# Kernel optimization log

Measured on AMD Instinct MI355X. Metric: run time of the kernel, lower is better.

The kernel has to match this reference:

```python
import jax, jax.numpy as jnp
import numpy as np

N = 50000        # nodes
E = 600000       # edges (no self-loops; reference adds N self-loops)
IN_C = 64
OUT_C = 64
HEADS = 2
NEG_SLOPE = 0.2  # GraphLayer default negative_slope
BN_EPS = 1e-5


def setup_inputs() -> dict:
    key = jax.random.key(0)
    ks = jax.random.split(key, 14)
    x = jax.random.normal(ks[0], (N, IN_C), dtype=jnp.float32)
    # edge_index with no self-loops by construction (original calls remove_self_loops)
    src = jax.random.randint(ks[1], (E,), 0, N, dtype=jnp.int32)
    off = jax.random.randint(ks[2], (E,), 1, N, dtype=jnp.int32)
    dst = (src + off) % N
    edge_index = jnp.stack([src, dst])  # [2, E]
    embedding = jax.random.normal(ks[3], (N, OUT_C), dtype=jnp.float32)
    s = 0.1
    lin_w = jax.random.normal(ks[4], (IN_C, HEADS * OUT_C), dtype=jnp.float32) * s
    att_i = jax.random.normal(ks[5], (1, HEADS, OUT_C), dtype=jnp.float32) * s
    att_j = jax.random.normal(ks[6], (1, HEADS, OUT_C), dtype=jnp.float32) * s
    att_em_i = jax.random.normal(ks[7], (1, HEADS, OUT_C), dtype=jnp.float32) * s
    att_em_j = jax.random.normal(ks[8], (1, HEADS, OUT_C), dtype=jnp.float32) * s
    gnn_bias = jnp.zeros((HEADS * OUT_C,), dtype=jnp.float32)
    ff_w = jax.random.normal(ks[9], (HEADS * OUT_C, OUT_C), dtype=jnp.float32) * s
    ff_b = jnp.zeros((OUT_C,), dtype=jnp.float32)
    bn_gamma = jnp.ones((OUT_C,), dtype=jnp.float32)
    bn_beta = jnp.zeros((OUT_C,), dtype=jnp.float32)
    return {"x": x, "edge_index": edge_index, "embedding": embedding,
            "lin_w": lin_w, "att_i": att_i, "att_j": att_j,
            "att_em_i": att_em_i, "att_em_j": att_em_j, "gnn_bias": gnn_bias,
            "ff_w": ff_w, "ff_b": ff_b, "bn_gamma": bn_gamma, "bn_beta": bn_beta}


def reference(x, edge_index, embedding, lin_w, att_i, att_j, att_em_i, att_em_j,
              gnn_bias, ff_w, ff_b, bn_gamma, bn_beta):
    n = x.shape[0]
    h = (x @ lin_w).reshape(n, HEADS, OUT_C)  # lin projection, per-head view
    # add self-loops (input already has none)
    ar = jnp.arange(n, dtype=edge_index.dtype)
    ei = jnp.concatenate([edge_index, jnp.stack([ar, ar])], axis=1)
    src, dst = ei[0], ei[1]                   # x_j = source, x_i = target
    x_i, x_j = h[dst], h[src]                 # [Et, H, C]
    emb_i = embedding[dst][:, None, :]        # [Et, 1, C] broadcast over heads
    emb_j = embedding[src][:, None, :]
    # alpha = <cat(x_i,emb_i), cat(att_i,att_em_i)> + <cat(x_j,emb_j), cat(att_j,att_em_j)>
    alpha = ((x_i * att_i[0]).sum(-1) + (emb_i * att_em_i[0]).sum(-1)
             + (x_j * att_j[0]).sum(-1) + (emb_j * att_em_j[0]).sum(-1))  # [Et, H]
    alpha = jax.nn.leaky_relu(alpha, NEG_SLOPE)
    # segment softmax over incoming edges of each target node (PyG softmax)
    amax = jax.ops.segment_max(alpha, dst, num_segments=n)
    ex = jnp.exp(alpha - amax[dst])
    denom = jax.ops.segment_sum(ex, dst, num_segments=n)
    alpha = ex / (denom[dst] + 1e-16)
    out = jax.ops.segment_sum(x_j * alpha[:, :, None], dst, num_segments=n)  # [n,H,C]
    out = out.reshape(n, HEADS * OUT_C) + gnn_bias  # concat heads + bias
    out = out @ ff_w + ff_b                         # self.ff
    mean = out.mean(axis=0)                          # BatchNorm1d, training stats
    var = out.var(axis=0)                            # biased variance (torch BN)
    out = (out - mean) / jnp.sqrt(var + BN_EPS) * bn_gamma + bn_beta
    return jax.nn.relu(out)
```

## Files before the change

### kernel.cpp

```cpp
#include <hip/hip_runtime.h>

#define C 64
#define HC 128
#define NEG 0.2f

typedef __attribute__((ext_vector_type(8))) short bf16x8;
typedef __attribute__((ext_vector_type(4))) float f32x4;

__device__ __forceinline__ float lrelu(float v) { return v >= 0.f ? v : NEG * v; }
__device__ __forceinline__ unsigned short f2bf(float f) {
    unsigned u = __float_as_uint(f);
    return (unsigned short)((u + 0x7fffu + ((u >> 16) & 1u)) >> 16);
}
__device__ __forceinline__ float bflo(unsigned u) { return __uint_as_float(u << 16); }
__device__ __forceinline__ float bfhi(unsigned u) { return __uint_as_float(u & 0xffff0000u); }

__global__ __launch_bounds__(256) void k1_mfma(
    const float* __restrict__ x, const float* __restrict__ lin_w,
    const float* __restrict__ emb,
    const float* __restrict__ att_i, const float* __restrict__ att_j,
    const float* __restrict__ att_em_i, const float* __restrict__ att_em_j,
    unsigned* __restrict__ hb, float2* __restrict__ a_i2,
    float2* __restrict__ a_j2, int n_nodes)
{
    __shared__ __align__(16) char smem[8192];
    const int t = threadIdx.x;
    const int lane = t & 63, w = t >> 6;
    const int r = lane & 15, g = lane >> 4;

    bf16x8 B[4][2][2];
#pragma unroll
    for (int m4 = 0; m4 < 4; ++m4)
#pragma unroll
        for (int p = 0; p < 2; ++p)
#pragma unroll
            for (int kk = 0; kk < 2; ++kk) {
                bf16x8 bb;
#pragma unroll
                for (int j = 0; j < 8; ++j)
                    bb[j] = (short)f2bf(lin_w[(kk * 32 + 8 * g + j) * HC + 32 * m4 + 2 * r + p]);
                B[m4][p][kk] = bb;
            }
    float wi[4][2], wj[4][2];
#pragma unroll
    for (int m4 = 0; m4 < 4; ++m4)
#pragma unroll
        for (int p = 0; p < 2; ++p) {
            wi[m4][p] = att_i[32 * m4 + 2 * r + p];
            wj[m4][p] = att_j[32 * m4 + 2 * r + p];
        }
    float wem_i0[4], wem_i1[4], wem_j0[4], wem_j1[4];
#pragma unroll
    for (int q = 0; q < 4; ++q) {
        wem_i0[q] = att_em_i[q * 16 + r];
        wem_i1[q] = att_em_i[64 + q * 16 + r];
        wem_j0[q] = att_em_j[q * 16 + r];
        wem_j1[q] = att_em_j[64 + q * 16 + r];
    }

    {
        const int row = t >> 2, q = t & 3;
        const int gn = blockIdx.x * 64 + row;
        float ff[16];
        if (gn < n_nodes) {
            const float4* xs = (const float4*)(x + (size_t)gn * C + q * 16);
            *(float4*)&ff[0] = xs[0]; *(float4*)&ff[4] = xs[1];
            *(float4*)&ff[8] = xs[2]; *(float4*)&ff[12] = xs[3];
        } else {
#pragma unroll
            for (int j = 0; j < 16; ++j) ff[j] = 0.f;
        }
        bf16x8 p0, p1;
#pragma unroll
        for (int j = 0; j < 8; ++j) {
            p0[j] = (short)f2bf(ff[j]);
            p1[j] = (short)f2bf(ff[8 + j]);
        }
        const unsigned bb = (unsigned)((row >> 4) * 2048 + (row & 15) * 128 + q * 32);
        const unsigned sw = (unsigned)((row & 7) << 4);
        *(bf16x8*)(smem + ((bb) ^ sw)) = p0;
        *(bf16x8*)(smem + ((bb + 16) ^ sw)) = p1;
    }
    __syncthreads();

    bf16x8 A[2];
    const unsigned ab = (unsigned)(w * 2048 + r * 128 + g * 16);
    const unsigned sw = (unsigned)((r & 7) << 4);
    A[0] = *(const bf16x8*)(smem + ((ab) ^ sw));
    A[1] = *(const bf16x8*)(smem + ((ab + 64) ^ sw));

    f32x4 acc[4][2];
#pragma unroll
    for (int m4 = 0; m4 < 4; ++m4)
#pragma unroll
        for (int p = 0; p < 2; ++p) acc[m4][p] = (f32x4){0.f, 0.f, 0.f, 0.f};
#pragma unroll
    for (int kk = 0; kk < 2; ++kk)
#pragma unroll
        for (int m4 = 0; m4 < 4; ++m4)
#pragma unroll
            for (int p = 0; p < 2; ++p)
                acc[m4][p] = __builtin_amdgcn_mfma_f32_16x16x32_bf16(A[kk], B[m4][p][kk], acc[m4][p], 0, 0, 0);

    const int nb = blockIdx.x * 64 + w * 16 + 4 * g;
#pragma unroll
    for (int j = 0; j < 4; ++j) {
        const int rr = nb + j;
        if (rr < n_nodes) {
            float pi0 = 0.f, pi1 = 0.f, pj0 = 0.f, pj1 = 0.f;
            unsigned* hp = hb + (size_t)rr * 64 + r;
#pragma unroll
            for (int m4 = 0; m4 < 4; ++m4) {
                const float ev = acc[m4][0][j], ov = acc[m4][1][j];
                hp[m4 * 16] = ((unsigned)f2bf(ov) << 16) | (unsigned)f2bf(ev);
                if (m4 < 2) {
                    pi0 = fmaf(ev, wi[m4][0], fmaf(ov, wi[m4][1], pi0));
                    pj0 = fmaf(ev, wj[m4][0], fmaf(ov, wj[m4][1], pj0));
                } else {
                    pi1 = fmaf(ev, wi[m4][0], fmaf(ov, wi[m4][1], pi1));
                    pj1 = fmaf(ev, wj[m4][0], fmaf(ov, wj[m4][1], pj1));
                }
            }
#pragma unroll
            for (int q = 0; q < 4; ++q) {
                const float ev = emb[(size_t)rr * C + q * 16 + r];
                pi0 = fmaf(ev, wem_i0[q], pi0);
                pi1 = fmaf(ev, wem_i1[q], pi1);
                pj0 = fmaf(ev, wem_j0[q], pj0);
                pj1 = fmaf(ev, wem_j1[q], pj1);
            }
#pragma unroll
            for (int m = 1; m < 16; m <<= 1) {
                pi0 += __shfl_xor(pi0, m, 64);
                pi1 += __shfl_xor(pi1, m, 64);
                pj0 += __shfl_xor(pj0, m, 64);
                pj1 += __shfl_xor(pj1, m, 64);
            }
            if (r == 0) {
                a_i2[rr] = make_float2(pi0, pi1);
                a_j2[rr] = make_float2(pj0, pj1);
            }
        }
    }
}

__global__ __launch_bounds__(256) void k_edge(
    const int* __restrict__ dstv, int* __restrict__ deg,
    int* __restrict__ rank, int e)
{
    int i = blockIdx.x * 256 + threadIdx.x;
    if (i < e) rank[i] = atomicAdd(&deg[dstv[i]], 1);
}

__global__ __launch_bounds__(256) void k_scan(
    const int* __restrict__ deg, int* __restrict__ counter,
    int* __restrict__ rowptr, int n)
{
    __shared__ int sh[256];
    __shared__ int s_base;
    const int t = threadIdx.x;
    const int i0 = blockIdx.x * 512 + t * 2;
    const int a = (i0 < n) ? deg[i0] : 0;
    const int b = (i0 + 1 < n) ? deg[i0 + 1] : 0;
    const int s = a + b;
    sh[t] = s;
    __syncthreads();
    for (int off = 1; off < 256; off <<= 1) {
        int v = (t >= off) ? sh[t - off] : 0;
        __syncthreads();
        sh[t] += v;
        __syncthreads();
    }
    const int excl = sh[t] - s;
    if (t == 255) s_base = atomicAdd(counter, sh[255]);
    __syncthreads();
    const int base = s_base;
    if (i0 < n)     rowptr[i0]     = base + excl;
    if (i0 + 1 < n) rowptr[i0 + 1] = base + excl + a;
}

__global__ __launch_bounds__(256) void k_fill(
    const int* __restrict__ srcv, const int* __restrict__ dstv,
    const int* __restrict__ rank, const int* __restrict__ rowptr,
    int* __restrict__ csr, int e)
{
    int i = blockIdx.x * 256 + threadIdx.x;
    if (i >= e) return;
    csr[rowptr[dstv[i]] + rank[i]] = srcv[i];
}

__global__ __launch_bounds__(256) void k_gather(
    const int* __restrict__ csr, const int* __restrict__ rowptr,
    const int* __restrict__ deg, const unsigned* __restrict__ hb,
    const float2* __restrict__ a_i2, const float2* __restrict__ a_j2,
    const float2* __restrict__ bias2, unsigned* __restrict__ out1b, int n_nodes)
{
    const int lane = threadIdx.x & 63;
    const int n = blockIdx.x * 4 + (threadIdx.x >> 6);
    if (n >= n_nodes) return;
    const int r0 = __builtin_amdgcn_readfirstlane(rowptr[n]);
    const int r1 = r0 + __builtin_amdgcn_readfirstlane(deg[n]);
    const float2 ai = a_i2[n];
    const float2 ajs = a_j2[n];
    const float es0 = __expf(lrelu(ai.x + ajs.x));
    const float es1 = __expf(lrelu(ai.y + ajs.y));
    float den0 = es0, den1 = es1;
    const unsigned hv = hb[(size_t)n * 64 + lane];
    const float exs = (lane < 32) ? es0 : es1;
    float2 acc = make_float2(exs * bflo(hv), exs * bfhi(hv));
#pragma unroll 4
    for (int r = r0; r < r1; ++r) {
        const int se = csr[r];
        const float2 aj = a_j2[se];
        const float ex0 = __expf(lrelu(ai.x + aj.x));
        const float ex1 = __expf(lrelu(ai.y + aj.y));
        den0 += ex0; den1 += ex1;
        const float exh = (lane < 32) ? ex0 : ex1;
        const unsigned v = hb[(size_t)se * 64 + lane];
        acc.x = fmaf(exh, bflo(v), acc.x);
        acc.y = fmaf(exh, bfhi(v), acc.y);
    }
    const float den = (lane < 32) ? den0 : den1;
    const float inv = 1.f / (den + 1e-16f);
    const float2 bv = bias2[lane];
    const unsigned lo = f2bf(fmaf(acc.x, inv, bv.x));
    const unsigned hi = f2bf(fmaf(acc.y, inv, bv.y));
    out1b[(size_t)n * 64 + lane] = (hi << 16) | lo;
}

__global__ __launch_bounds__(256) void k4_ff(
    const unsigned* __restrict__ out1b, const float* __restrict__ ff_w,
    const float* __restrict__ ff_b, float* __restrict__ out2,
    float* __restrict__ colsum, float* __restrict__ colsq, int n_nodes)
{
    __shared__ __align__(16) char smem[16384];
    const int t = threadIdx.x;
    const int lane = t & 63, w = t >> 6;
    const int r = lane & 15, g = lane >> 4;

    bf16x8 B[4][4];
#pragma unroll
    for (int tt = 0; tt < 4; ++tt)
#pragma unroll
        for (int kk = 0; kk < 4; ++kk) {
            bf16x8 bb;
#pragma unroll
            for (int j = 0; j < 8; ++j)
                bb[j] = (short)f2bf(ff_w[(kk * 32 + 8 * g + j) * C + tt * 16 + r]);
            B[tt][kk] = bb;
        }
    float fb[4];
#pragma unroll
    for (int tt = 0; tt < 4; ++tt) fb[tt] = ff_b[tt * 16 + r];

    {
        const int row = t >> 2, q = t & 3;
        const int gn = blockIdx.x * 64 + row;
        uint4 u[4];
        if (gn < n_nodes) {
            const uint4* rs = (const uint4*)(out1b + (size_t)gn * 64 + q * 16);
            u[0] = rs[0]; u[1] = rs[1]; u[2] = rs[2]; u[3] = rs[3];
        } else {
            u[0] = u[1] = u[2] = u[3] = make_uint4(0, 0, 0, 0);
        }
        const unsigned bb = (unsigned)((row >> 4) * 4096 + (row & 15) * 256 + q * 64);
        const unsigned sw = (unsigned)((row & 7) << 4);
#pragma unroll
        for (int i2 = 0; i2 < 4; ++i2)
            *(uint4*)(smem + ((bb + i2 * 16) ^ sw)) = u[i2];
    }
    __syncthreads();

    bf16x8 A[4];
    const unsigned ab = (unsigned)(w * 4096 + r * 256 + g * 16);
    const unsigned sw = (unsigned)((r & 7) << 4);
#pragma unroll
    for (int kk = 0; kk < 4; ++kk)
        A[kk] = *(const bf16x8*)(smem + ((ab + kk * 64) ^ sw));

    f32x4 acc[4];
#pragma unroll
    for (int tt = 0; tt < 4; ++tt) acc[tt] = (f32x4){0.f, 0.f, 0.f, 0.f};
#pragma unroll
    for (int kk = 0; kk < 4; ++kk)
#pragma unroll
        for (int tt = 0; tt < 4; ++tt)
            acc[tt] = __builtin_amdgcn_mfma_f32_16x16x32_bf16(A[kk], B[tt][kk], acc[tt], 0, 0, 0);

    const int nb = blockIdx.x * 64 + w * 16 + 4 * g;
    float st[4] = {0.f, 0.f, 0.f, 0.f}, st2[4] = {0.f, 0.f, 0.f, 0.f};
#pragma unroll
    for (int j = 0; j < 4; ++j) {
        const int rr = nb + j;
        if (rr < n_nodes) {
            float* op = out2 + (size_t)rr * C + r;
#pragma unroll
            for (int tt = 0; tt < 4; ++tt) {
                const float v = acc[tt][j] + fb[tt];
                op[tt * 16] = v;
                st[tt] += v;
                st2[tt] = fmaf(v, v, st2[tt]);
            }
        }
    }
#pragma unroll
    for (int tt = 0; tt < 4; ++tt) {
        st[tt]  += __shfl_xor(st[tt], 16, 64);
        st[tt]  += __shfl_xor(st[tt], 32, 64);
        st2[tt] += __shfl_xor(st2[tt], 16, 64);
        st2[tt] += __shfl_xor(st2[tt], 32, 64);
    }
    __syncthreads();
    float* sred = (float*)smem;
    if (g == 0) {
#pragma unroll
        for (int tt = 0; tt < 4; ++tt) {
            sred[w * 64 + tt * 16 + r]       = st[tt];
            sred[256 + w * 64 + tt * 16 + r] = st2[tt];
        }
    }
    __syncthreads();
    if (t < C) {
        const float s  = sred[t] + sred[64 + t] + sred[128 + t] + sred[192 + t];
        const float s2 = sred[256 + t] + sred[320 + t] + sred[384 + t] + sred[448 + t];
        atomicAdd(&colsum[t], s);
        atomicAdd(&colsq[t], s2);
    }
}

__global__ __launch_bounds__(256) void k6_bn(
    float* __restrict__ out2, const float* __restrict__ colsum,
    const float* __restrict__ colsq, const float* __restrict__ gamma,
    const float* __restrict__ beta, float inv_n, int total )
{
    int i = blockIdx.x * 256 + threadIdx.x;
    if (i >= total) return;
    int c = i & 63;
    float mean = colsum[c] * inv_n;
    float var = colsq[c] * inv_n - mean * mean;
    float rstd = rsqrtf(var + 1e-5f);
    float v = (out2[i] - mean) * rstd * gamma[c] + beta[c];
    out2[i] = fmaxf(v, 0.f);
}

extern "C" void kernel_launch(void* const* d_in, const int* in_sizes, int n_in,
                              void* d_out, int out_size, void* d_ws, size_t ws_size,
                              hipStream_t stream)
{
    const float* x        = (const float*)d_in[0];
    const int*   ei       = (const int*)d_in[1];
    const float* emb      = (const float*)d_in[2];
    const float* lin_w    = (const float*)d_in[3];
    const float* att_i    = (const float*)d_in[4];
    const float* att_j    = (const float*)d_in[5];
    const float* att_em_i = (const float*)d_in[6];
    const float* att_em_j = (const float*)d_in[7];
    const float* gnn_bias = (const float*)d_in[8];
    const float* ff_w     = (const float*)d_in[9];
    const float* ff_b     = (const float*)d_in[10];
    const float* bn_g     = (const float*)d_in[11];
    const float* bn_b     = (const float*)d_in[12];

    const int n = in_sizes[0] / C;
    const int e = in_sizes[1] / 2;
    const int* srcv = ei;
    const int* dstv = ei + e;

    float* ws = (float*)d_ws;
    unsigned* hb      = (unsigned*)ws;
    float*    a_if    = (float*)(hb + (size_t)n * 64);
    float*    a_jf    = a_if + 2 * (size_t)n;
    unsigned* out1b   = (unsigned*)(a_jf + 2 * (size_t)n);
    float*    colsum  = (float*)(out1b + (size_t)n * 64);
    float*    colsq   = colsum + C;
    int*      deg     = (int*)(colsq + C);
    int*      counter = deg + n;
    int*      rowptr  = counter + 1;
    int*      rank    = rowptr + n;
    int*      csr     = rank + e;
    float*    out2    = (float*)d_out;

    hipMemsetAsync(colsum, 0, (size_t)(2 * C + n + 1) * sizeof(float), stream);

    const int nb64 = (n + 63) / 64;
    k1_mfma<<<nb64, 256, 0, stream>>>(x, lin_w, emb, att_i, att_j,
                                      att_em_i, att_em_j, hb,
                                      (float2*)a_if, (float2*)a_jf, n);
    k_edge<<<(e + 255) / 256, 256, 0, stream>>>(dstv, deg, rank, e);
    k_scan<<<(n + 511) / 512, 256, 0, stream>>>(deg, counter, rowptr, n);
    k_fill<<<(e + 255) / 256, 256, 0, stream>>>(srcv, dstv, rank, rowptr, csr, e);
    k_gather<<<(n + 3) / 4, 256, 0, stream>>>(csr, rowptr, deg, hb,
                                              (const float2*)a_if,
                                              (const float2*)a_jf,
                                              (const float2*)gnn_bias,
                                              out1b, n);
    k4_ff<<<nb64, 256, 0, stream>>>(out1b, ff_w, ff_b, out2, colsum, colsq, n);
    {
        int total = n * C;
        k6_bn<<<(total + 255) / 256, 256, 0, stream>>>(out2, colsum, colsq, bn_g, bn_b,
                                                       1.0f / (float)n, total);
    }
}
```

Before: 218.8 us.

## Fuse edge counting into projection, fuse gather with FF GEMM, deterministic BN reduction

```diff
diff --git a/kernel.cpp b/kernel.cpp
--- a/kernel.cpp
+++ b/kernel.cpp
@@ -15,16 +15,23 @@
 __device__ __forceinline__ float bflo(unsigned u) { return __uint_as_float(u << 16); }
 __device__ __forceinline__ float bfhi(unsigned u) { return __uint_as_float(u & 0xffff0000u); }
 
-__global__ __launch_bounds__(256) void k1_mfma(
+__global__ __launch_bounds__(256) void kA_mfma_edge(
     const float* __restrict__ x, const float* __restrict__ lin_w,
     const float* __restrict__ emb,
     const float* __restrict__ att_i, const float* __restrict__ att_j,
     const float* __restrict__ att_em_i, const float* __restrict__ att_em_j,
     unsigned* __restrict__ hb, float2* __restrict__ a_i2,
-    float2* __restrict__ a_j2, int n_nodes)
-{
+    float2* __restrict__ a_j2, int n_nodes, int nb64,
+    const int* __restrict__ dstv, int* __restrict__ deg,
+    int* __restrict__ rank, int e)
+{
+    const int t = threadIdx.x;
+    if (blockIdx.x >= nb64) {
+        const int i = (blockIdx.x - nb64) * 256 + t;
+        if (i < e) rank[i] = atomicAdd(&deg[dstv[i]], 1);
+        return;
+    }
     __shared__ __align__(16) char smem[8192];
-    const int t = threadIdx.x;
     const int lane = t & 63, w = t >> 6;
     const int r = lane & 15, g = lane >> 4;
 
@@ -144,14 +151,6 @@
     }
 }
 
-__global__ __launch_bounds__(256) void k_edge(
-    const int* __restrict__ dstv, int* __restrict__ deg,
-    int* __restrict__ rank, int e)
-{
-    int i = blockIdx.x * 256 + threadIdx.x;
-    if (i < e) rank[i] = atomicAdd(&deg[dstv[i]], 1);
-}
-
 __global__ __launch_bounds__(256) void k_scan(
     const int* __restrict__ deg, int* __restrict__ counter,
     int* __restrict__ rowptr, int n)
@@ -189,142 +188,117 @@
     csr[rowptr[dstv[i]] + rank[i]] = srcv[i];
 }
 
-__global__ __launch_bounds__(256) void k_gather(
+__global__ __launch_bounds__(256) void kD_gff(
     const int* __restrict__ csr, const int* __restrict__ rowptr,
     const int* __restrict__ deg, const unsigned* __restrict__ hb,
     const float2* __restrict__ a_i2, const float2* __restrict__ a_j2,
-    const float2* __restrict__ bias2, unsigned* __restrict__ out1b, int n_nodes)
-{
-    const int lane = threadIdx.x & 63;
-    const int n = blockIdx.x * 4 + (threadIdx.x >> 6);
-    if (n >= n_nodes) return;
-    const int r0 = __builtin_amdgcn_readfirstlane(rowptr[n]);
-    const int r1 = r0 + __builtin_amdgcn_readfirstlane(deg[n]);
-    const float2 ai = a_i2[n];
-    const float2 ajs = a_j2[n];
-    const float es0 = __expf(lrelu(ai.x + ajs.x));
-    const float es1 = __expf(lrelu(ai.y + ajs.y));
-    float den0 = es0, den1 = es1;
-    const unsigned hv = hb[(size_t)n * 64 + lane];
-    const float exs = (lane < 32) ? es0 : es1;
-    float2 acc = make_float2(exs * bflo(hv), exs * bfhi(hv));
-#pragma unroll 4
-    for (int r = r0; r < r1; ++r) {
-        const int se = csr[r];
-        const float2 aj = a_j2[se];
-        const float ex0 = __expf(lrelu(ai.x + aj.x));
-        const float ex1 = __expf(lrelu(ai.y + aj.y));
-        den0 += ex0; den1 += ex1;
-        const float exh = (lane < 32) ? ex0 : ex1;
-        const unsigned v = hb[(size_t)se * 64 + lane];
-        acc.x = fmaf(exh, bflo(v), acc.x);
-        acc.y = fmaf(exh, bfhi(v), acc.y);
-    }
-    const float den = (lane < 32) ? den0 : den1;
-    const float inv = 1.f / (den + 1e-16f);
-    const float2 bv = bias2[lane];
-    const unsigned lo = f2bf(fmaf(acc.x, inv, bv.x));
-    const unsigned hi = f2bf(fmaf(acc.y, inv, bv.y));
-    out1b[(size_t)n * 64 + lane] = (hi << 16) | lo;
-}
-
-__global__ __launch_bounds__(256) void k4_ff(
-    const unsigned* __restrict__ out1b, const float* __restrict__ ff_w,
+    const float2* __restrict__ bias2, const float* __restrict__ ff_w,
     const float* __restrict__ ff_b, float* __restrict__ out2,
-    float* __restrict__ colsum, float* __restrict__ colsq, int n_nodes)
-{
-    __shared__ __align__(16) char smem[16384];
+    float* __restrict__ partial, int n_nodes)
+{
+    __shared__ __align__(16) char smem[4096];
     const int t = threadIdx.x;
     const int lane = t & 63, w = t >> 6;
     const int r = lane & 15, g = lane >> 4;
 
-    bf16x8 B[4][4];
-#pragma unroll
-    for (int tt = 0; tt < 4; ++tt)
-#pragma unroll
-        for (int kk = 0; kk < 4; ++kk) {
-            bf16x8 bb;
-#pragma unroll
-            for (int j = 0; j < 8; ++j)
-                bb[j] = (short)f2bf(ff_w[(kk * 32 + 8 * g + j) * C + tt * 16 + r]);
-            B[tt][kk] = bb;
-        }
-    float fb[4];
-#pragma unroll
-    for (int tt = 0; tt < 4; ++tt) fb[tt] = ff_b[tt * 16 + r];
-
-    {
-        const int row = t >> 2, q = t & 3;
-        const int gn = blockIdx.x * 64 + row;
-        uint4 u[4];
-        if (gn < n_nodes) {
-            const uint4* rs = (const uint4*)(out1b + (size_t)gn * 64 + q * 16);
-            u[0] = rs[0]; u[1] = rs[1]; u[2] = rs[2]; u[3] = rs[3];
-        } else {
-            u[0] = u[1] = u[2] = u[3] = make_uint4(0, 0, 0, 0);
-        }
-        const unsigned bb = (unsigned)((row >> 4) * 4096 + (row & 15) * 256 + q * 64);
-        const unsigned sw = (unsigned)((row & 7) << 4);
-#pragma unroll
-        for (int i2 = 0; i2 < 4; ++i2)
-            *(uint4*)(smem + ((bb + i2 * 16) ^ sw)) = u[i2];
+    bf16x8 B[4];
+#pragma unroll
+    for (int kk = 0; kk < 4; ++kk) {
+        bf16x8 bb;
+#pragma unroll
+        for (int j = 0; j < 8; ++j)
+            bb[j] = (short)f2bf(ff_w[(kk * 32 + 8 * g + j) * C + w * 16 + r]);
+        B[kk] = bb;
+    }
+    const float fb = ff_b[w * 16 + r];
+    const float2 bv = bias2[lane];
+
+    const int nbase = blockIdx.x * 16;
+#pragma unroll
+    for (int j = 0; j < 4; ++j) {
+        const int n = nbase + w * 4 + j;
+        unsigned packed = 0;
+        if (n < n_nodes) {
+            const int r0 = __builtin_amdgcn_readfirstlane(rowptr[n]);
+            const int r1 = r0 + __builtin_amdgcn_readfirstlane(deg[n]);
+            const float2 ai = a_i2[n];
+            const float2 ajs = a_j2[n];
+            const float es0 = __expf(lrelu(ai.x + ajs.x));
+            const float es1 = __expf(lrelu(ai.y + ajs.y));
+            float den0 = es0, den1 = es1;
+            const unsigned hv = hb[(size_t)n * 64 + lane];
+            const float exs = (lane < 32) ? es0 : es1;
+            float2 acc = make_float2(exs * bflo(hv), exs * bfhi(hv));
+#pragma unroll 4
+            for (int rr = r0; rr < r1; ++rr) {
+                const int se = csr[rr];
+                const float2 aj = a_j2[se];
+                const float ex0 = __expf(lrelu(ai.x + aj.x));
+                const float ex1 = __expf(lrelu(ai.y + aj.y));
+                den0 += ex0; den1 += ex1;
+                const float exh = (lane < 32) ? ex0 : ex1;
+                const unsigned v = hb[(size_t)se * 64 + lane];
+                acc.x = fmaf(exh, bflo(v), acc.x);
+                acc.y = fmaf(exh, bfhi(v), acc.y);
+            }
+            const float den = (lane < 32) ? den0 : den1;
+            const float inv = 1.f / (den + 1e-16f);
+            packed = ((unsigned)f2bf(fmaf(acc.y, inv, bv.y)) << 16)
+                   | (unsigned)f2bf(fmaf(acc.x, inv, bv.x));
+        }
+        const int row = w * 4 + j;
+        const unsigned byte = (unsigned)(row * 256 + lane * 4);
+        *(unsigned*)(smem + (byte ^ ((unsigned)(row & 7) << 4))) = packed;
     }
     __syncthreads();
 
     bf16x8 A[4];
-    const unsigned ab = (unsigned)(w * 4096 + r * 256 + g * 16);
-    const unsigned sw = (unsigned)((r & 7) << 4);
+#pragma unroll
+    for (int kk = 0; kk < 4; ++kk) {
+        const unsigned byte = (unsigned)(r * 256 + kk * 64 + g * 16);
+        A[kk] = *(const bf16x8*)(smem + (byte ^ ((unsigned)(r & 7) << 4)));
+    }
+    f32x4 acc4 = (f32x4){0.f, 0.f, 0.f, 0.f};
 #pragma unroll
     for (int kk = 0; kk < 4; ++kk)
-        A[kk] = *(const bf16x8*)(smem + ((ab + kk * 64) ^ sw));
-
-    f32x4 acc[4];
-#pragma unroll
-    for (int tt = 0; tt < 4; ++tt) acc[tt] = (f32x4){0.f, 0.f, 0.f, 0.f};
-#pragma unroll
-    for (int kk = 0; kk < 4; ++kk)
-#pragma unroll
-        for (int tt = 0; tt < 4; ++tt)
-            acc[tt] = __builtin_amdgcn_mfma_f32_16x16x32_bf16(A[kk], B[tt][kk], acc[tt], 0, 0, 0);
-
-    const int nb = blockIdx.x * 64 + w * 16 + 4 * g;
-    float st[4] = {0.f, 0.f, 0.f, 0.f}, st2[4] = {0.f, 0.f, 0.f, 0.f};
-#pragma unroll
-    for (int j = 0; j < 4; ++j) {
-        const int rr = nb + j;
+        acc4 = __builtin_amdgcn_mfma_f32_16x16x32_bf16(A[kk], B[kk], acc4, 0, 0, 0);
+
+    float st = 0.f, st2 = 0.f;
+#pragma unroll
+    for (int jj = 0; jj < 4; ++jj) {
+        const int rr = nbase + 4 * g + jj;
         if (rr < n_nodes) {
-            float* op = out2 + (size_t)rr * C + r;
-#pragma unroll
-            for (int tt = 0; tt < 4; ++tt) {
-                const float v = acc[tt][j] + fb[tt];
-                op[tt * 16] = v;
-                st[tt] += v;
-                st2[tt] = fmaf(v, v, st2[tt]);
-            }
-        }
-    }
-#pragma unroll
-    for (int tt = 0; tt < 4; ++tt) {
-        st[tt]  += __shfl_xor(st[tt], 16, 64);
-        st[tt]  += __shfl_xor(st[tt], 32, 64);
-        st2[tt] += __shfl_xor(st2[tt], 16, 64);
-        st2[tt] += __shfl_xor(st2[tt], 32, 64);
-    }
-    __syncthreads();
-    float* sred = (float*)smem;
+            const float v = acc4[jj] + fb;
+            out2[(size_t)rr * C + w * 16 + r] = v;
+            st += v; st2 = fmaf(v, v, st2);
+        }
+    }
+    st  += __shfl_xor(st, 16, 64);  st  += __shfl_xor(st, 32, 64);
+    st2 += __shfl_xor(st2, 16, 64); st2 += __shfl_xor(st2, 32, 64);
     if (g == 0) {
-#pragma unroll
-        for (int tt = 0; tt < 4; ++tt) {
-            sred[w * 64 + tt * 16 + r]       = st[tt];
-            sred[256 + w * 64 + tt * 16 + r] = st2[tt];
-        }
-    }
-    __syncthreads();
-    if (t < C) {
-        const float s  = sred[t] + sred[64 + t] + sred[128 + t] + sred[192 + t];
-        const float s2 = sred[256 + t] + sred[320 + t] + sred[384 + t] + sred[448 + t];
-        atomicAdd(&colsum[t], s);
-        atomicAdd(&colsq[t], s2);
+        partial[(size_t)blockIdx.x * 128 + w * 16 + r] = st;
+        partial[(size_t)blockIdx.x * 128 + 64 + w * 16 + r] = st2;
+    }
+}
+
+__global__ __launch_bounds__(256) void k5_red(
+    const float* __restrict__ partial, float* __restrict__ colsum,
+    float* __restrict__ colsq, int nblk)
+{
+    __shared__ float sh[256];
+    const int c = blockIdx.x;
+    const int t = threadIdx.x;
+    float s = 0.f;
+    for (int b = t; b < nblk; b += 256) s += partial[(size_t)b * 128 + c];
+    sh[t] = s;
+    __syncthreads();
+    for (int off = 128; off; off >>= 1) {
+        if (t < off) sh[t] += sh[t + off];
+        __syncthreads();
+    }
+    if (t == 0) {
+        if (c < C) colsum[c] = sh[0];
+        else       colsq[c - C] = sh[0];
     }
 }
 
@@ -366,12 +340,16 @@
     const int* srcv = ei;
     const int* dstv = ei + e;
 
+    const int nb64  = (n + 63) / 64;
+    const int nb16  = (n + 15) / 16;
+    const int nbE   = (e + 255) / 256;
+
     float* ws = (float*)d_ws;
     unsigned* hb      = (unsigned*)ws;
     float*    a_if    = (float*)(hb + (size_t)n * 64);
     float*    a_jf    = a_if + 2 * (size_t)n;
-    unsigned* out1b   = (unsigned*)(a_jf + 2 * (size_t)n);
-    float*    colsum  = (float*)(out1b + (size_t)n * 64);
+    float*    partial = a_jf + 2 * (size_t)n;
+    float*    colsum  = partial + (size_t)nb16 * 128;
     float*    colsq   = colsum + C;
     int*      deg     = (int*)(colsq + C);
     int*      counter = deg + n;
@@ -380,21 +358,18 @@
     int*      csr     = rank + e;
     float*    out2    = (float*)d_out;
 
-    hipMemsetAsync(colsum, 0, (size_t)(2 * C + n + 1) * sizeof(float), stream);
-
-    const int nb64 = (n + 63) / 64;
-    k1_mfma<<<nb64, 256, 0, stream>>>(x, lin_w, emb, att_i, att_j,
-                                      att_em_i, att_em_j, hb,
-                                      (float2*)a_if, (float2*)a_jf, n);
-    k_edge<<<(e + 255) / 256, 256, 0, stream>>>(dstv, deg, rank, e);
+    hipMemsetAsync(deg, 0, (size_t)(n + 1) * sizeof(int), stream);
+
+    kA_mfma_edge<<<nb64 + nbE, 256, 0, stream>>>(
+        x, lin_w, emb, att_i, att_j, att_em_i, att_em_j,
+        hb, (float2*)a_if, (float2*)a_jf, n, nb64, dstv, deg, rank, e);
     k_scan<<<(n + 511) / 512, 256, 0, stream>>>(deg, counter, rowptr, n);
-    k_fill<<<(e + 255) / 256, 256, 0, stream>>>(srcv, dstv, rank, rowptr, csr, e);
-    k_gather<<<(n + 3) / 4, 256, 0, stream>>>(csr, rowptr, deg, hb,
-                                              (const float2*)a_if,
-                                              (const float2*)a_jf,
-                                              (const float2*)gnn_bias,
-                                              out1b, n);
-    k4_ff<<<nb64, 256, 0, stream>>>(out1b, ff_w, ff_b, out2, colsum, colsq, n);
+    k_fill<<<nbE, 256, 0, stream>>>(srcv, dstv, rank, rowptr, csr, e);
+    kD_gff<<<nb16, 256, 0, stream>>>(csr, rowptr, deg, hb,
+                                     (const float2*)a_if, (const float2*)a_jf,
+                                     (const float2*)gnn_bias, ff_w, ff_b,
+                                     out2, partial, n);
+    k5_red<<<128, 256, 0, stream>>>(partial, colsum, colsq, nb16);
     {
         int total = n * C;
         k6_bn<<<(total + 255) / 256, 256, 0, stream>>>(out2, colsum, colsq, bn_g, bn_b,
```

After: 201.9 us. -7.7%, faster.
